# Optimization experiments

Hardware: AMD Instinct MI355X
Metric: run time of the kernel (lower is better)

## Reference

```python
import jax, jax.numpy as jnp
import numpy as np

B, S, D, H = 4, 2048, 1024, 16
HD = D // H
SCALE = D ** (-0.5)  # NOTE: original scales by embedding_dim**-0.5, not head_size**-0.5


def setup_inputs() -> dict:
    key = jax.random.key(0)
    k1, k2, k3, k4, k5 = jax.random.split(key, 5)
    return {
        "x": jax.random.normal(k1, (B, S, D), dtype=jnp.float32),
        "Wqkv": jax.random.normal(k2, (3 * D, D), dtype=jnp.float32) * (D ** -0.5),
        "bqkv": jax.random.normal(k3, (3 * D,), dtype=jnp.float32) * 0.02,
        "Wlift": jax.random.normal(k4, (D, D), dtype=jnp.float32) * (D ** -0.5),
        "blift": jax.random.normal(k5, (D,), dtype=jnp.float32) * 0.02,
    }


def reference(x, Wqkv, bqkv, Wlift, blift):
    b, s, d = x.shape
    # qkv projection -> (b, s, 3, H, HD) -> (3, b, H, s, HD)
    qkv = (x @ Wqkv.T + bqkv).reshape(b, s, 3, H, HD).transpose(2, 0, 3, 1, 4)
    q, k, v = qkv[0], qkv[1], qkv[2]  # each (b, H, s, HD)
    # full score matrix, softmax over keys
    scores = jnp.einsum("bhqd,bhkd->bhqk", q, k) * SCALE
    a = jax.nn.softmax(scores, axis=-1)
    # post-hoc causal mask + renormalize (as in the original)
    a = jnp.tril(a)
    a = a / jnp.sum(a, axis=-1, keepdims=True)
    attn = jnp.einsum("bhqk,bhkd->bhqd", a, v)  # (b, H, s, HD)
    attn = attn.swapaxes(1, 2).reshape(b, s, d)  # (b, s, d)
    # lifting linear; Dropout(0.2) is identity in eval mode
    return attn @ Wlift.T + blift
```

## Files before the change

kernel.cpp:

```cpp
#include <hip/hip_runtime.h>
#include <cstdint>
#include <cstddef>

typedef unsigned short u16;
typedef unsigned int u32;
typedef __bf16 bf16x8 __attribute__((ext_vector_type(8)));
typedef float f32x4 __attribute__((ext_vector_type(4)));
typedef float f32x16 __attribute__((ext_vector_type(16)));

__device__ __forceinline__ u16 f2bf(float f) {
  unsigned u = __builtin_bit_cast(unsigned, f);
  return (u16)((u + 0x7FFFu + ((u >> 16) & 1u)) >> 16);
}

__device__ __forceinline__ u32 pk2bf(float lo, float hi) {
  union { __bf16 h[2]; u32 u; } t;
  t.h[0] = (__bf16)lo; t.h[1] = (__bf16)hi;
  return t.u;
}

__device__ __forceinline__ void gl_lds16(const void* g, void* l) {
  __builtin_amdgcn_global_load_lds(
      (const __attribute__((address_space(1))) unsigned int*)g,
      (__attribute__((address_space(3))) unsigned int*)l,
      16, 0, 0);
}

__global__ void cast4_kernel(const float* __restrict__ in, u16* __restrict__ out, int n4) {
  int i = blockIdx.x * blockDim.x + threadIdx.x;
  if (i < n4) {
    float4 v = reinterpret_cast<const float4*>(in)[i];
    ushort4 o;
    o.x = f2bf(v.x); o.y = f2bf(v.y); o.z = f2bf(v.z); o.w = f2bf(v.w);
    reinterpret_cast<ushort4*>(out)[i] = o;
  }
}

template <int EPI>
__global__ __launch_bounds__(256)
void gemm_bt_kernel(const u16* __restrict__ A, const u16* __restrict__ Bw,
                    const float* __restrict__ bias,
                    u16* __restrict__ oq, u16* __restrict__ ok, u16* __restrict__ ovT,
                    float* __restrict__ ofp, int M, int N, int K) {
  __shared__ __align__(16) u16 Als[2][128 * 32];
  __shared__ __align__(16) u16 Bls[2][128 * 32];

  const int tid = threadIdx.x;
  const int lane = tid & 63;
  const int w = tid >> 6, wr = w >> 1, wc = w & 1;
  const int lr = lane & 15, lk = lane >> 4;
  const int brow = blockIdx.y * 128, bcol = blockIdx.x * 128;

  const int srow = tid >> 2;
  const int scol = (tid & 3) << 3;
  const u16* ga = A + (size_t)(brow + srow) * K + scol;
  const u16* gb = Bw + (size_t)(bcol + srow) * K + scol;

  f32x4 acc[4][4] = {};

  auto stage = [&](int buf, int kt) {
    const u16* a0 = ga + kt * 32;
    const u16* b0 = gb + kt * 32;
    gl_lds16(a0,             &Als[buf][tid * 8]);
    gl_lds16(a0 + 64 * K,    &Als[buf][2048 + tid * 8]);
    gl_lds16(b0,             &Bls[buf][tid * 8]);
    gl_lds16(b0 + 64 * K,    &Bls[buf][2048 + tid * 8]);
  };

  stage(0, 0);
  __syncthreads();

  const int nt = K >> 5;
  int cur = 0;
  for (int t = 0; t < nt; ++t) {
    if (t + 1 < nt) stage(cur ^ 1, t + 1);
    bf16x8 af[4], bfr[4];
#pragma unroll
    for (int m = 0; m < 4; ++m)
      af[m] = *reinterpret_cast<const bf16x8*>(&Als[cur][(wr * 64 + m * 16 + lr) * 32 + lk * 8]);
#pragma unroll
    for (int n = 0; n < 4; ++n)
      bfr[n] = *reinterpret_cast<const bf16x8*>(&Bls[cur][(wc * 64 + n * 16 + lr) * 32 + lk * 8]);
#pragma unroll
    for (int m = 0; m < 4; ++m)
#pragma unroll
      for (int n = 0; n < 4; ++n)
        acc[m][n] = __builtin_amdgcn_mfma_f32_16x16x32_bf16(af[m], bfr[n], acc[m][n], 0, 0, 0);
    __syncthreads();
    cur ^= 1;
  }

  if (EPI == 0) {
    const int three = bcol >> 10;
#pragma unroll
    for (int n = 0; n < 4; ++n) {
      const int c = bcol + wc * 64 + n * 16 + lr;
      const float bv = bias[c];
      const int cc = c & 1023, h = cc >> 6, hd = cc & 63;
#pragma unroll
      for (int m = 0; m < 4; ++m) {
        const int r0 = brow + wr * 64 + m * 16 + lk * 4;
        const int b = r0 >> 11;
        const int s0 = r0 & 2047;
        if (three == 2) {
          ushort4 pkv;
          pkv.x = f2bf(acc[m][n][0] + bv);
          pkv.y = f2bf(acc[m][n][1] + bv);
          pkv.z = f2bf(acc[m][n][2] + bv);
          pkv.w = f2bf(acc[m][n][3] + bv);
          *reinterpret_cast<ushort4*>(&ovT[((size_t)(b * 16 + h) * 64 + hd) * 2048 + s0]) = pkv;
        } else {
          u16* dst = (three == 0) ? oq : ok;
          const float sc = (three == 0) ? 0.03125f * 1.44269504089f : 1.0f;
#pragma unroll
          for (int j = 0; j < 4; ++j)
            dst[((size_t)(b * 16 + h) * 2048 + (s0 + j)) * 64 + hd] = f2bf((acc[m][n][j] + bv) * sc);
        }
      }
    }
  } else {
#pragma unroll
    for (int n = 0; n < 4; ++n) {
      const int c = bcol + wc * 64 + n * 16 + lr;
      const float bv = bias[c];
#pragma unroll
      for (int m = 0; m < 4; ++m) {
        const int r0 = brow + wr * 64 + m * 16 + lk * 4;
#pragma unroll
        for (int j = 0; j < 4; ++j)
          ofp[(size_t)(r0 + j) * N + c] = acc[m][n][j] + bv;
      }
    }
  }
}

__global__ __launch_bounds__(512, 4)
void attn_causal_kernel(const u16* __restrict__ qg, const u16* __restrict__ kg_,
                        const u16* __restrict__ vT, u16* __restrict__ ob) {
  __shared__ __align__(16) u16 Kls[2][64 * 64];
  __shared__ __align__(16) u16 Vls[2][64 * 64];

  const int tid = threadIdx.x, lane = tid & 63, w = tid >> 6;
  const int n = lane & 31, hi = lane >> 5;
  const int bid = blockIdx.x;
  const int bh = bid & 63;
  const int qb = (bid < 256) ? (7 - (bid >> 6)) : ((bid - 256) >> 6);
  const int q0w = qb * 256 + w * 32;
  const size_t base = (size_t)bh * 2048 * 64;
  const size_t vbase = (size_t)bh * 64 * 2048;

  bf16x8 qf[4];
#pragma unroll
  for (int dc = 0; dc < 4; ++dc)
    qf[dc] = *reinterpret_cast<const bf16x8*>(
        &qg[base + (size_t)(q0w + n) * 64 + dc * 16 + hi * 8]);

  f32x16 o0 = {}, o1 = {};
  float l = 0.f;

  const int ktiles = qb * 4 + 4;

  const int krow = tid >> 3, kch = tid & 7;
  const int szr = (krow ^ (krow >> 3)) & 7;
  const u16* kgp = kg_ + base + (size_t)krow * 64 + (kch ^ szr) * 8;
  const u16* vgp = vT + vbase + (size_t)krow * 2048 + (kch ^ szr) * 8;

  auto stage = [&](int buf, int t) {
    gl_lds16(kgp + (size_t)t * 4096, &Kls[buf][tid * 8]);
    gl_lds16(vgp + t * 64,           &Vls[buf][tid * 8]);
  };

  const int sw0 = ((n ^ (n >> 3)) & 7) << 4;
  const int sw1 = (((32 + n) ^ ((32 + n) >> 3)) & 7) << 4;

  stage(0, 0);
  __syncthreads();

  int cur = 0;
  for (int t = 0; t < ktiles; ++t) {
    const int k0 = t << 6;
    if (t + 1 < ktiles) stage(cur ^ 1, t + 1);
    if (k0 <= q0w) {
      const char* Kb = (const char*)&Kls[cur][0];
      const char* Vb = (const char*)&Vls[cur][0];
      const bool act1 = (k0 + 32) <= q0w;

      f32x16 st0 = {}, st1 = {};
      __builtin_amdgcn_s_setprio(1);
#pragma unroll
      for (int dc = 0; dc < 4; ++dc) {
        bf16x8 kf = *reinterpret_cast<const bf16x8*>(
            Kb + n * 128 + ((((dc << 1) | hi) << 4) ^ sw0));
        st0 = __builtin_amdgcn_mfma_f32_32x32x16_bf16(kf, qf[dc], st0, 0, 0, 0);
      }
      if (act1) {
#pragma unroll
        for (int dc = 0; dc < 4; ++dc) {
          bf16x8 kf = *reinterpret_cast<const bf16x8*>(
              Kb + (32 + n) * 128 + ((((dc << 1) | hi) << 4) ^ sw1));
          st1 = __builtin_amdgcn_mfma_f32_32x32x16_bf16(kf, qf[dc], st1, 0, 0, 0);
        }
      }
      __builtin_amdgcn_s_setprio(0);

      if (k0 == q0w) {
#pragma unroll
        for (int r = 0; r < 16; ++r) {
          const int koff = (r & 3) + 8 * (r >> 2) + 4 * hi;
          if (koff > n) st0[r] = -1e30f;
        }
      }
      if (act1 && (k0 + 32) == q0w) {
#pragma unroll
        for (int r = 0; r < 16; ++r) {
          const int koff = (r & 3) + 8 * (r >> 2) + 4 * hi;
          if (koff > n) st1[r] = -1e30f;
        }
      }

      float rs = 0.f;
#pragma unroll
      for (int r = 0; r < 16; ++r) { st0[r] = __builtin_amdgcn_exp2f(st0[r]); rs += st0[r]; }
      if (act1) {
#pragma unroll
        for (int r = 0; r < 16; ++r) { st1[r] = __builtin_amdgcn_exp2f(st1[r]); rs += st1[r]; }
      }
      l += rs;

      union { u32 u[4]; bf16x8 v; } pb[4];
#pragma unroll
      for (int s = 0; s < 2; ++s) {
        if (s == 1 && !act1) break;
        const f32x16& st = s ? st1 : st0;
#pragma unroll
        for (int kk = 0; kk < 2; ++kk) {
          const int gown = (kk * 2 + hi) * 4, gsnd = (kk * 2 + (hi ^ 1)) * 4;
          u32 pa0 = pk2bf(st[gown + 0], st[gown + 1]);
          u32 pa1 = pk2bf(st[gown + 2], st[gown + 3]);
          u32 ps0 = pk2bf(st[gsnd + 0], st[gsnd + 1]);
          u32 ps1 = pk2bf(st[gsnd + 2], st[gsnd + 3]);
          u32 rA = __shfl_xor(ps0, 32, 64);
          u32 rB = __shfl_xor(ps1, 32, 64);
          pb[s * 2 + kk].u[0] = hi ? rA : pa0;
          pb[s * 2 + kk].u[1] = hi ? rB : pa1;
          pb[s * 2 + kk].u[2] = hi ? pa0 : rA;
          pb[s * 2 + kk].u[3] = hi ? pa1 : rB;
        }
      }
      __builtin_amdgcn_s_setprio(1);
#pragma unroll
      for (int s = 0; s < 2; ++s) {
        if (s == 1 && !act1) break;
#pragma unroll
        for (int kk = 0; kk < 2; ++kk) {
          const int c = ((s * 4 + kk * 2 + hi) << 4);
          bf16x8 vf0 = *reinterpret_cast<const bf16x8*>(Vb + n * 128 + (c ^ sw0));
          o0 = __builtin_amdgcn_mfma_f32_32x32x16_bf16(vf0, pb[s * 2 + kk].v, o0, 0, 0, 0);
          bf16x8 vf1 = *reinterpret_cast<const bf16x8*>(Vb + (32 + n) * 128 + (c ^ sw1));
          o1 = __builtin_amdgcn_mfma_f32_32x32x16_bf16(vf1, pb[s * 2 + kk].v, o1, 0, 0, 0);
        }
      }
      __builtin_amdgcn_s_setprio(0);
    }
    __syncthreads();
    cur ^= 1;
  }

  const int b = bh >> 4, h = bh & 15;
  const float lt = l + __shfl_xor(l, 32, 64);
  const float inv = 1.f / lt;
  const size_t rbase = ((size_t)(b * 2048 + q0w + n)) * 1024 + h * 64;
#pragma unroll
  for (int g = 0; g < 4; ++g) {
    ushort4 w0, w1;
    w0.x = f2bf(o0[g * 4 + 0] * inv); w0.y = f2bf(o0[g * 4 + 1] * inv);
    w0.z = f2bf(o0[g * 4 + 2] * inv); w0.w = f2bf(o0[g * 4 + 3] * inv);
    w1.x = f2bf(o1[g * 4 + 0] * inv); w1.y = f2bf(o1[g * 4 + 1] * inv);
    w1.z = f2bf(o1[g * 4 + 2] * inv); w1.w = f2bf(o1[g * 4 + 3] * inv);
    *reinterpret_cast<ushort4*>(&ob[rbase + g * 8 + hi * 4]) = w0;
    *reinterpret_cast<ushort4*>(&ob[rbase + 32 + g * 8 + hi * 4]) = w1;
  }
}

extern "C" void kernel_launch(void* const* d_in, const int* in_sizes, int n_in,
                              void* d_out, int out_size, void* d_ws, size_t ws_size,
                              hipStream_t stream) {
  const float* x     = (const float*)d_in[0];
  const float* Wqkv  = (const float*)d_in[1];
  const float* bqkv  = (const float*)d_in[2];
  const float* Wlift = (const float*)d_in[3];
  const float* blift = (const float*)d_in[4];
  float* out = (float*)d_out;

  if (ws_size < 40ull * 1024 * 1024) return;

  char* ws = (char*)d_ws;
  u16* xb     = (u16*)(ws);
  u16* wqkvb  = (u16*)(ws + 16777216);
  u16* wliftb = (u16*)(ws + 23068672);
  u16* vT     = (u16*)(ws + 25165824);
  u16* attnb  = xb;
  u16* qb = (u16*)d_out;
  u16* kb = qb + 8388608;

  cast4_kernel<<<8192, 256, 0, stream>>>(x, xb, 2097152);
  cast4_kernel<<<3072, 256, 0, stream>>>(Wqkv, wqkvb, 786432);
  cast4_kernel<<<1024, 256, 0, stream>>>(Wlift, wliftb, 262144);

  gemm_bt_kernel<0><<<dim3(24, 64), 256, 0, stream>>>(
      xb, wqkvb, bqkv, qb, kb, vT, nullptr, 8192, 3072, 1024);

  attn_causal_kernel<<<512, 512, 0, stream>>>(qb, kb, vT, attnb);

  gemm_bt_kernel<1><<<dim3(8, 64), 256, 0, stream>>>(
      attnb, wliftb, blift, nullptr, nullptr, nullptr, out, 8192, 1024, 1024);
}
```

Baseline: 299.8 us.

## Stage K/V tiles through registers with two-ahead prefetch instead of direct-to-LDS loads

Replaces the direct global-to-LDS async copies of K and V tiles with ordinary global loads into registers, issued two tiles ahead. Each tile is written into the swizzled LDS slot after the current tile's compute finishes. The old __syncthreads becomes an explicit lgkmcnt wait, s_barrier and sched_barrier. The aim is to hide global-load latency behind more than one tile of MFMA work, at the cost of extra VGPRs for the staging buffers and explicit LDS stores on the critical path.

```diff
diff --git a/kernel.cpp b/kernel.cpp
--- a/kernel.cpp
+++ b/kernel.cpp
@@ -162,27 +162,35 @@
 
   const int krow = tid >> 3, kch = tid & 7;
   const int szr = (krow ^ (krow >> 3)) & 7;
-  const u16* kgp = kg_ + base + (size_t)krow * 64 + (kch ^ szr) * 8;
-  const u16* vgp = vT + vbase + (size_t)krow * 2048 + (kch ^ szr) * 8;
-
-  auto stage = [&](int buf, int t) {
-    gl_lds16(kgp + (size_t)t * 4096, &Kls[buf][tid * 8]);
-    gl_lds16(vgp + t * 64,           &Vls[buf][tid * 8]);
-  };
+  const u16* kgp = kg_ + base + (size_t)krow * 64 + kch * 8;
+  const u16* vgp = vT + vbase + (size_t)krow * 2048 + kch * 8;
+  u16* kwp = &Kls[0][krow * 64 + (kch ^ szr) * 8];
+  u16* vwp = &Vls[0][krow * 64 + (kch ^ szr) * 8];
+
+  int4 kst[2], vst[2];
+  kst[0] = *reinterpret_cast<const int4*>(kgp);
+  vst[0] = *reinterpret_cast<const int4*>(vgp);
+  kst[1] = *reinterpret_cast<const int4*>(kgp + 4096);
+  vst[1] = *reinterpret_cast<const int4*>(vgp + 64);
+  *reinterpret_cast<int4*>(kwp) = kst[0];
+  *reinterpret_cast<int4*>(vwp) = vst[0];
+  asm volatile("s_waitcnt lgkmcnt(0)" ::: "memory");
+  __builtin_amdgcn_s_barrier();
+  __builtin_amdgcn_sched_barrier(0);
 
   const int sw0 = ((n ^ (n >> 3)) & 7) << 4;
   const int sw1 = (((32 + n) ^ ((32 + n) >> 3)) & 7) << 4;
 
-  stage(0, 0);
-  __syncthreads();
-
-  int cur = 0;
   for (int t = 0; t < ktiles; ++t) {
     const int k0 = t << 6;
-    if (t + 1 < ktiles) stage(cur ^ 1, t + 1);
+    const int slot = t & 1;
+    if (t + 2 < ktiles) {
+      kst[slot] = *reinterpret_cast<const int4*>(kgp + (size_t)(t + 2) * 4096);
+      vst[slot] = *reinterpret_cast<const int4*>(vgp + (t + 2) * 64);
+    }
     if (k0 <= q0w) {
-      const char* Kb = (const char*)&Kls[cur][0];
-      const char* Vb = (const char*)&Vls[cur][0];
+      const char* Kb = (const char*)&Kls[slot][0];
+      const char* Vb = (const char*)&Vls[slot][0];
       const bool act1 = (k0 + 32) <= q0w;
 
       f32x16 st0 = {}, st1 = {};
@@ -262,8 +270,14 @@
       }
       __builtin_amdgcn_s_setprio(0);
     }
-    __syncthreads();
-    cur ^= 1;
+    if (t + 1 < ktiles) {
+      const int ws = (t + 1) & 1;
+      *reinterpret_cast<int4*>(kwp + ws * 4096) = kst[ws];
+      *reinterpret_cast<int4*>(vwp + ws * 4096) = vst[ws];
+    }
+    asm volatile("s_waitcnt lgkmcnt(0)" ::: "memory");
+    __builtin_amdgcn_s_barrier();
+    __builtin_amdgcn_sched_barrier(0);
   }
 
   const int b = bh >> 4, h = bh & 15;
```

Measured after the change: 324.5 us. 8.2% more time.

## Pair mirrored query strips per wave and stage K/V through registers

Applied to the files above, without the earlier changes.

Each wave now owns two 32-row query strips (j and 63-j), so every block does the same causal work. Each block streams all 32 K/V tiles once and shares them across both strips. The async global-to-LDS loads are replaced by register-staged loads with a two-deep prefetch and explicit barriers, and the block size drops from 512 to 256 threads. This targets load imbalance across blocks and K/V reload overhead, at the cost of more live registers (two Q fragment sets and accumulators) and lower per-block parallelism.

```diff
diff --git a/kernel.cpp b/kernel.cpp
--- a/kernel.cpp
+++ b/kernel.cpp
@@ -134,7 +134,7 @@
   }
 }
 
-__global__ __launch_bounds__(512, 4)
+__global__ __launch_bounds__(256, 2)
 void attn_causal_kernel(const u16* __restrict__ qg, const u16* __restrict__ kg_,
                         const u16* __restrict__ vT, u16* __restrict__ ob) {
   __shared__ __align__(16) u16 Kls[2][64 * 64];
@@ -144,142 +144,175 @@
   const int n = lane & 31, hi = lane >> 5;
   const int bid = blockIdx.x;
   const int bh = bid & 63;
-  const int qb = (bid < 256) ? (7 - (bid >> 6)) : ((bid - 256) >> 6);
-  const int q0w = qb * 256 + w * 32;
+  const int bq = bid >> 6;
+  const int jA = bq * 4 + w;
+  const int jB = 63 - jA;
+  const int q0A = jA * 32, q0B = jB * 32;
   const size_t base = (size_t)bh * 2048 * 64;
   const size_t vbase = (size_t)bh * 64 * 2048;
 
-  bf16x8 qf[4];
-#pragma unroll
-  for (int dc = 0; dc < 4; ++dc)
-    qf[dc] = *reinterpret_cast<const bf16x8*>(
-        &qg[base + (size_t)(q0w + n) * 64 + dc * 16 + hi * 8]);
-
-  f32x16 o0 = {}, o1 = {};
-  float l = 0.f;
-
-  const int ktiles = qb * 4 + 4;
-
-  const int krow = tid >> 3, kch = tid & 7;
-  const int szr = (krow ^ (krow >> 3)) & 7;
-  const u16* kgp = kg_ + base + (size_t)krow * 64 + (kch ^ szr) * 8;
-  const u16* vgp = vT + vbase + (size_t)krow * 2048 + (kch ^ szr) * 8;
-
-  auto stage = [&](int buf, int t) {
-    gl_lds16(kgp + (size_t)t * 4096, &Kls[buf][tid * 8]);
-    gl_lds16(vgp + t * 64,           &Vls[buf][tid * 8]);
-  };
+  bf16x8 qfA[4], qfB[4];
+#pragma unroll
+  for (int dc = 0; dc < 4; ++dc) {
+    qfA[dc] = *reinterpret_cast<const bf16x8*>(
+        &qg[base + (size_t)(q0A + n) * 64 + dc * 16 + hi * 8]);
+    qfB[dc] = *reinterpret_cast<const bf16x8*>(
+        &qg[base + (size_t)(q0B + n) * 64 + dc * 16 + hi * 8]);
+  }
+
+  f32x16 oA0 = {}, oA1 = {}, oB0 = {}, oB1 = {};
+  float lA = 0.f, lB = 0.f;
+
+  const int srow_ = tid >> 2;
+  const int sch = tid & 3;
+  const int ssz = (srow_ ^ (srow_ >> 3)) & 7;
+  const u16* kgp = kg_ + base + (size_t)srow_ * 64 + sch * 8;
+  const u16* vgp = vT + vbase + (size_t)srow_ * 2048 + sch * 8;
+  u16* kw0 = &Kls[0][srow_ * 64 + ((sch ^ ssz) * 8)];
+  u16* kw1 = &Kls[0][srow_ * 64 + (((sch + 4) ^ ssz) * 8)];
+  u16* vw0 = &Vls[0][srow_ * 64 + ((sch ^ ssz) * 8)];
+  u16* vw1 = &Vls[0][srow_ * 64 + (((sch + 4) ^ ssz) * 8)];
 
   const int sw0 = ((n ^ (n >> 3)) & 7) << 4;
   const int sw1 = (((32 + n) ^ ((32 + n) >> 3)) & 7) << 4;
 
-  stage(0, 0);
-  __syncthreads();
-
-  int cur = 0;
-  for (int t = 0; t < ktiles; ++t) {
-    const int k0 = t << 6;
-    if (t + 1 < ktiles) stage(cur ^ 1, t + 1);
-    if (k0 <= q0w) {
-      const char* Kb = (const char*)&Kls[cur][0];
-      const char* Vb = (const char*)&Vls[cur][0];
-      const bool act1 = (k0 + 32) <= q0w;
-
-      f32x16 st0 = {}, st1 = {};
+  struct Slot { int4 k0, k1, v0, v1; };
+  Slot sA, sB;
+
+  sA.k0 = *reinterpret_cast<const int4*>(kgp);
+  sA.k1 = *reinterpret_cast<const int4*>(kgp + 32);
+  sA.v0 = *reinterpret_cast<const int4*>(vgp);
+  sA.v1 = *reinterpret_cast<const int4*>(vgp + 32);
+  sB.k0 = *reinterpret_cast<const int4*>(kgp + 4096);
+  sB.k1 = *reinterpret_cast<const int4*>(kgp + 4096 + 32);
+  sB.v0 = *reinterpret_cast<const int4*>(vgp + 64);
+  sB.v1 = *reinterpret_cast<const int4*>(vgp + 64 + 32);
+  *reinterpret_cast<int4*>(kw0) = sA.k0;
+  *reinterpret_cast<int4*>(kw1) = sA.k1;
+  *reinterpret_cast<int4*>(vw0) = sA.v0;
+  *reinterpret_cast<int4*>(vw1) = sA.v1;
+  asm volatile("s_waitcnt lgkmcnt(0)" ::: "memory");
+  __builtin_amdgcn_s_barrier();
+  __builtin_amdgcn_sched_barrier(0);
+
+  auto slab_one = [&](const char* Kb, const char* Vb, int s, bool diag,
+                      const bf16x8 (&qf)[4], f32x16& o0, f32x16& o1, float& l) {
+    const int swK = s ? sw1 : sw0;
+    f32x16 st = {};
+    __builtin_amdgcn_s_setprio(1);
+#pragma unroll
+    for (int dc = 0; dc < 4; ++dc) {
+      bf16x8 kf = *reinterpret_cast<const bf16x8*>(
+          Kb + (s * 32 + n) * 128 + ((((dc << 1) | hi) << 4) ^ swK));
+      st = __builtin_amdgcn_mfma_f32_32x32x16_bf16(kf, qf[dc], st, 0, 0, 0);
+    }
+    __builtin_amdgcn_s_setprio(0);
+    if (diag) {
+#pragma unroll
+      for (int r = 0; r < 16; ++r) {
+        const int koff = (r & 3) + 8 * (r >> 2) + 4 * hi;
+        if (koff > n) st[r] = -1e30f;
+      }
+    }
+    float rs = 0.f;
+#pragma unroll
+    for (int r = 0; r < 16; ++r) { st[r] = __builtin_amdgcn_exp2f(st[r]); rs += st[r]; }
+    l += rs;
+#pragma unroll
+    for (int kk = 0; kk < 2; ++kk) {
+      const int gown = (kk * 2 + hi) * 4, gsnd = (kk * 2 + (hi ^ 1)) * 4;
+      u32 pa0 = pk2bf(st[gown + 0], st[gown + 1]);
+      u32 pa1 = pk2bf(st[gown + 2], st[gown + 3]);
+      u32 ps0 = pk2bf(st[gsnd + 0], st[gsnd + 1]);
+      u32 ps1 = pk2bf(st[gsnd + 2], st[gsnd + 3]);
+      u32 rA = __shfl_xor(ps0, 32, 64);
+      u32 rB = __shfl_xor(ps1, 32, 64);
+      union { u32 u[4]; bf16x8 v; } pb;
+      pb.u[0] = hi ? rA : pa0;
+      pb.u[1] = hi ? rB : pa1;
+      pb.u[2] = hi ? pa0 : rA;
+      pb.u[3] = hi ? pa1 : rB;
+      const int c = ((s * 4 + kk * 2 + hi) << 4);
       __builtin_amdgcn_s_setprio(1);
-#pragma unroll
-      for (int dc = 0; dc < 4; ++dc) {
-        bf16x8 kf = *reinterpret_cast<const bf16x8*>(
-            Kb + n * 128 + ((((dc << 1) | hi) << 4) ^ sw0));
-        st0 = __builtin_amdgcn_mfma_f32_32x32x16_bf16(kf, qf[dc], st0, 0, 0, 0);
-      }
-      if (act1) {
-#pragma unroll
-        for (int dc = 0; dc < 4; ++dc) {
-          bf16x8 kf = *reinterpret_cast<const bf16x8*>(
-              Kb + (32 + n) * 128 + ((((dc << 1) | hi) << 4) ^ sw1));
-          st1 = __builtin_amdgcn_mfma_f32_32x32x16_bf16(kf, qf[dc], st1, 0, 0, 0);
-        }
-      }
+      bf16x8 vf0 = *reinterpret_cast<const bf16x8*>(Vb + n * 128 + (c ^ sw0));
+      o0 = __builtin_amdgcn_mfma_f32_32x32x16_bf16(vf0, pb.v, o0, 0, 0, 0);
+      bf16x8 vf1 = *reinterpret_cast<const bf16x8*>(Vb + (32 + n) * 128 + (c ^ sw1));
+      o1 = __builtin_amdgcn_mfma_f32_32x32x16_bf16(vf1, pb.v, o1, 0, 0, 0);
       __builtin_amdgcn_s_setprio(0);
-
-      if (k0 == q0w) {
-#pragma unroll
-        for (int r = 0; r < 16; ++r) {
-          const int koff = (r & 3) + 8 * (r >> 2) + 4 * hi;
-          if (koff > n) st0[r] = -1e30f;
-        }
-      }
-      if (act1 && (k0 + 32) == q0w) {
-#pragma unroll
-        for (int r = 0; r < 16; ++r) {
-          const int koff = (r & 3) + 8 * (r >> 2) + 4 * hi;
-          if (koff > n) st1[r] = -1e30f;
-        }
-      }
-
-      float rs = 0.f;
-#pragma unroll
-      for (int r = 0; r < 16; ++r) { st0[r] = __builtin_amdgcn_exp2f(st0[r]); rs += st0[r]; }
-      if (act1) {
-#pragma unroll
-        for (int r = 0; r < 16; ++r) { st1[r] = __builtin_amdgcn_exp2f(st1[r]); rs += st1[r]; }
-      }
-      l += rs;
-
-      union { u32 u[4]; bf16x8 v; } pb[4];
-#pragma unroll
-      for (int s = 0; s < 2; ++s) {
-        if (s == 1 && !act1) break;
-        const f32x16& st = s ? st1 : st0;
-#pragma unroll
-        for (int kk = 0; kk < 2; ++kk) {
-          const int gown = (kk * 2 + hi) * 4, gsnd = (kk * 2 + (hi ^ 1)) * 4;
-          u32 pa0 = pk2bf(st[gown + 0], st[gown + 1]);
-          u32 pa1 = pk2bf(st[gown + 2], st[gown + 3]);
-          u32 ps0 = pk2bf(st[gsnd + 0], st[gsnd + 1]);
-          u32 ps1 = pk2bf(st[gsnd + 2], st[gsnd + 3]);
-          u32 rA = __shfl_xor(ps0, 32, 64);
-          u32 rB = __shfl_xor(ps1, 32, 64);
-          pb[s * 2 + kk].u[0] = hi ? rA : pa0;
-          pb[s * 2 + kk].u[1] = hi ? rB : pa1;
-          pb[s * 2 + kk].u[2] = hi ? pa0 : rA;
-          pb[s * 2 + kk].u[3] = hi ? pa1 : rB;
-        }
-      }
-      __builtin_amdgcn_s_setprio(1);
-#pragma unroll
-      for (int s = 0; s < 2; ++s) {
-        if (s == 1 && !act1) break;
-#pragma unroll
-        for (int kk = 0; kk < 2; ++kk) {
-          const int c = ((s * 4 + kk * 2 + hi) << 4);
-          bf16x8 vf0 = *reinterpret_cast<const bf16x8*>(Vb + n * 128 + (c ^ sw0));
-          o0 = __builtin_amdgcn_mfma_f32_32x32x16_bf16(vf0, pb[s * 2 + kk].v, o0, 0, 0, 0);
-          bf16x8 vf1 = *reinterpret_cast<const bf16x8*>(Vb + (32 + n) * 128 + (c ^ sw1));
-          o1 = __builtin_amdgcn_mfma_f32_32x32x16_bf16(vf1, pb[s * 2 + kk].v, o1, 0, 0, 0);
-        }
-      }
-      __builtin_amdgcn_s_setprio(0);
-    }
-    __syncthreads();
-    cur ^= 1;
+    }
+  };
+
+  auto tilecomp = [&](int t, const char* Kb, const char* Vb) {
+#pragma unroll
+    for (int s = 0; s < 2; ++s) {
+      const int e = 2 * t + s;
+      if (e <= jA) slab_one(Kb, Vb, s, e == jA, qfA, oA0, oA1, lA);
+      if (e <= jB) slab_one(Kb, Vb, s, e == jB, qfB, oB0, oB1, lB);
+    }
+  };
+
+  const char* K0 = (const char*)&Kls[0][0];
+  const char* V0 = (const char*)&Vls[0][0];
+  const char* K1 = (const char*)&Kls[1][0];
+  const char* V1 = (const char*)&Vls[1][0];
+
+  for (int tp = 0; tp < 16; ++tp) {
+    {
+      const int t = tp * 2;
+      if (t + 2 < 32) {
+        sA.k0 = *reinterpret_cast<const int4*>(kgp + (size_t)(t + 2) * 4096);
+        sA.k1 = *reinterpret_cast<const int4*>(kgp + (size_t)(t + 2) * 4096 + 32);
+        sA.v0 = *reinterpret_cast<const int4*>(vgp + (t + 2) * 64);
+        sA.v1 = *reinterpret_cast<const int4*>(vgp + (t + 2) * 64 + 32);
+      }
+      tilecomp(t, K0, V0);
+      *reinterpret_cast<int4*>(kw0 + 4096) = sB.k0;
+      *reinterpret_cast<int4*>(kw1 + 4096) = sB.k1;
+      *reinterpret_cast<int4*>(vw0 + 4096) = sB.v0;
+      *reinterpret_cast<int4*>(vw1 + 4096) = sB.v1;
+      asm volatile("s_waitcnt lgkmcnt(0)" ::: "memory");
+      __builtin_amdgcn_s_barrier();
+      __builtin_amdgcn_sched_barrier(0);
+    }
+    {
+      const int t = tp * 2 + 1;
+      if (t + 2 < 32) {
+        sB.k0 = *reinterpret_cast<const int4*>(kgp + (size_t)(t + 2) * 4096);
+        sB.k1 = *reinterpret_cast<const int4*>(kgp + (size_t)(t + 2) * 4096 + 32);
+        sB.v0 = *reinterpret_cast<const int4*>(vgp + (t + 2) * 64);
+        sB.v1 = *reinterpret_cast<const int4*>(vgp + (t + 2) * 64 + 32);
+      }
+      tilecomp(t, K1, V1);
+      if (t + 1 < 32) {
+        *reinterpret_cast<int4*>(kw0) = sA.k0;
+        *reinterpret_cast<int4*>(kw1) = sA.k1;
+        *reinterpret_cast<int4*>(vw0) = sA.v0;
+        *reinterpret_cast<int4*>(vw1) = sA.v1;
+      }
+      asm volatile("s_waitcnt lgkmcnt(0)" ::: "memory");
+      __builtin_amdgcn_s_barrier();
+      __builtin_amdgcn_sched_barrier(0);
+    }
   }
 
   const int b = bh >> 4, h = bh & 15;
-  const float lt = l + __shfl_xor(l, 32, 64);
-  const float inv = 1.f / lt;
-  const size_t rbase = ((size_t)(b * 2048 + q0w + n)) * 1024 + h * 64;
-#pragma unroll
-  for (int g = 0; g < 4; ++g) {
-    ushort4 w0, w1;
-    w0.x = f2bf(o0[g * 4 + 0] * inv); w0.y = f2bf(o0[g * 4 + 1] * inv);
-    w0.z = f2bf(o0[g * 4 + 2] * inv); w0.w = f2bf(o0[g * 4 + 3] * inv);
-    w1.x = f2bf(o1[g * 4 + 0] * inv); w1.y = f2bf(o1[g * 4 + 1] * inv);
-    w1.z = f2bf(o1[g * 4 + 2] * inv); w1.w = f2bf(o1[g * 4 + 3] * inv);
-    *reinterpret_cast<ushort4*>(&ob[rbase + g * 8 + hi * 4]) = w0;
-    *reinterpret_cast<ushort4*>(&ob[rbase + 32 + g * 8 + hi * 4]) = w1;
-  }
+  auto epi = [&](int q0, const f32x16& o0, const f32x16& o1, float l) {
+    const float lt = l + __shfl_xor(l, 32, 64);
+    const float inv = 1.f / lt;
+    const size_t rbase = ((size_t)(b * 2048 + q0 + n)) * 1024 + h * 64;
+#pragma unroll
+    for (int g = 0; g < 4; ++g) {
+      ushort4 w0, w1;
+      w0.x = f2bf(o0[g * 4 + 0] * inv); w0.y = f2bf(o0[g * 4 + 1] * inv);
+      w0.z = f2bf(o0[g * 4 + 2] * inv); w0.w = f2bf(o0[g * 4 + 3] * inv);
+      w1.x = f2bf(o1[g * 4 + 0] * inv); w1.y = f2bf(o1[g * 4 + 1] * inv);
+      w1.z = f2bf(o1[g * 4 + 2] * inv); w1.w = f2bf(o1[g * 4 + 3] * inv);
+      *reinterpret_cast<ushort4*>(&ob[rbase + g * 8 + hi * 4]) = w0;
+      *reinterpret_cast<ushort4*>(&ob[rbase + 32 + g * 8 + hi * 4]) = w1;
+    }
+  };
+  epi(q0A, oA0, oA1, lA);
+  epi(q0B, oB0, oB1, lB);
 }
 
 extern "C" void kernel_launch(void* const* d_in, const int* in_sizes, int n_in,
@@ -310,7 +343,7 @@
   gemm_bt_kernel<0><<<dim3(24, 64), 256, 0, stream>>>(
       xb, wqkvb, bqkv, qb, kb, vT, nullptr, 8192, 3072, 1024);
 
-  attn_causal_kernel<<<512, 512, 0, stream>>>(qb, kb, vT, attnb);
+  attn_causal_kernel<<<512, 256, 0, stream>>>(qb, kb, vT, attnb);
 
   gemm_bt_kernel<1><<<dim3(8, 64), 256, 0, stream>>>(
       attnb, wliftb, blift, nullptr, nullptr, nullptr, out, 8192, 1024, 1024);
```

Result: slower. 322.8 us (+7.7%).

## Pair complementary causal query tiles per wave for balanced attention work

Applied to the files above, without the earlier changes.

Each wave now owns two 32-row query tiles, jA and 63-jA, so every wave does the same amount of causal work. Blocks shrink to 256 threads, and each block now streams all 32 K/V tiles for its head. Loaded K fragments are reused across both query tiles' MFMAs. The cost is more registers for two sets of accumulators, and each block now reads the full K/V sequence.

```diff
diff --git a/kernel.cpp b/kernel.cpp
--- a/kernel.cpp
+++ b/kernel.cpp
@@ -134,7 +134,7 @@
   }
 }
 
-__global__ __launch_bounds__(512, 4)
+__global__ __launch_bounds__(256, 2)
 void attn_causal_kernel(const u16* __restrict__ qg, const u16* __restrict__ kg_,
                         const u16* __restrict__ vT, u16* __restrict__ ob) {
   __shared__ __align__(16) u16 Kls[2][64 * 64];
@@ -144,30 +144,38 @@
   const int n = lane & 31, hi = lane >> 5;
   const int bid = blockIdx.x;
   const int bh = bid & 63;
-  const int qb = (bid < 256) ? (7 - (bid >> 6)) : ((bid - 256) >> 6);
-  const int q0w = qb * 256 + w * 32;
+  const int bq = bid >> 6;
+  const int jA = bq * 4 + w;
+  const int jB = 63 - jA;
+  const int q0A = jA * 32, q0B = jB * 32;
   const size_t base = (size_t)bh * 2048 * 64;
   const size_t vbase = (size_t)bh * 64 * 2048;
 
-  bf16x8 qf[4];
-#pragma unroll
-  for (int dc = 0; dc < 4; ++dc)
-    qf[dc] = *reinterpret_cast<const bf16x8*>(
-        &qg[base + (size_t)(q0w + n) * 64 + dc * 16 + hi * 8]);
-
-  f32x16 o0 = {}, o1 = {};
-  float l = 0.f;
-
-  const int ktiles = qb * 4 + 4;
+  bf16x8 qfA[4], qfB[4];
+#pragma unroll
+  for (int dc = 0; dc < 4; ++dc) {
+    qfA[dc] = *reinterpret_cast<const bf16x8*>(
+        &qg[base + (size_t)(q0A + n) * 64 + dc * 16 + hi * 8]);
+    qfB[dc] = *reinterpret_cast<const bf16x8*>(
+        &qg[base + (size_t)(q0B + n) * 64 + dc * 16 + hi * 8]);
+  }
+
+  f32x16 oA0 = {}, oA1 = {}, oB0 = {}, oB1 = {};
+  float lA = 0.f, lB = 0.f;
 
   const int krow = tid >> 3, kch = tid & 7;
-  const int szr = (krow ^ (krow >> 3)) & 7;
-  const u16* kgp = kg_ + base + (size_t)krow * 64 + (kch ^ szr) * 8;
-  const u16* vgp = vT + vbase + (size_t)krow * 2048 + (kch ^ szr) * 8;
 
   auto stage = [&](int buf, int t) {
-    gl_lds16(kgp + (size_t)t * 4096, &Kls[buf][tid * 8]);
-    gl_lds16(vgp + t * 64,           &Vls[buf][tid * 8]);
+    const int k0 = t << 6;
+#pragma unroll
+    for (int p = 0; p < 2; ++p) {
+      const int r = p * 32 + krow;
+      const int sz = (r ^ (r >> 3)) & 7;
+      gl_lds16(kg_ + base + (size_t)(k0 + r) * 64 + (kch ^ sz) * 8,
+               &Kls[buf][p * 2048 + tid * 8]);
+      gl_lds16(vT + vbase + (size_t)r * 2048 + k0 + (kch ^ sz) * 8,
+               &Vls[buf][p * 2048 + tid * 8]);
+    }
   };
 
   const int sw0 = ((n ^ (n >> 3)) & 7) << 4;
@@ -176,110 +184,114 @@
   stage(0, 0);
   __syncthreads();
 
-  int cur = 0;
-  for (int t = 0; t < ktiles; ++t) {
-    const int k0 = t << 6;
-    if (t + 1 < ktiles) stage(cur ^ 1, t + 1);
-    if (k0 <= q0w) {
-      const char* Kb = (const char*)&Kls[cur][0];
-      const char* Vb = (const char*)&Vls[cur][0];
-      const bool act1 = (k0 + 32) <= q0w;
-
-      f32x16 st0 = {}, st1 = {};
+  union U { u32 u[4]; bf16x8 v; };
+
+  auto maskst = [&](f32x16& st) {
+#pragma unroll
+    for (int r = 0; r < 16; ++r) {
+      const int koff = (r & 3) + 8 * (r >> 2) + 4 * hi;
+      if (koff > n) st[r] = -1e30f;
+    }
+  };
+  auto packp = [&](const f32x16& st, int kk, U& pb) {
+    const int gown = (kk * 2 + hi) * 4, gsnd = (kk * 2 + (hi ^ 1)) * 4;
+    u32 pa0 = pk2bf(st[gown + 0], st[gown + 1]);
+    u32 pa1 = pk2bf(st[gown + 2], st[gown + 3]);
+    u32 ps0 = pk2bf(st[gsnd + 0], st[gsnd + 1]);
+    u32 ps1 = pk2bf(st[gsnd + 2], st[gsnd + 3]);
+    u32 rA = __shfl_xor(ps0, 32, 64);
+    u32 rB = __shfl_xor(ps1, 32, 64);
+    pb.u[0] = hi ? rA : pa0;
+    pb.u[1] = hi ? rB : pa1;
+    pb.u[2] = hi ? pa0 : rA;
+    pb.u[3] = hi ? pa1 : rB;
+  };
+
+  auto slab_pair = [&](const char* Kb, const char* Vb, int s,
+                       bool actA, bool actB, bool diagA, bool diagB) {
+    const int swK = s ? sw1 : sw0;
+    bf16x8 kf[4];
+#pragma unroll
+    for (int dc = 0; dc < 4; ++dc)
+      kf[dc] = *reinterpret_cast<const bf16x8*>(
+          Kb + (s * 32 + n) * 128 + ((((dc << 1) | hi) << 4) ^ swK));
+    f32x16 stA = {}, stB = {};
+    __builtin_amdgcn_s_setprio(1);
+#pragma unroll
+    for (int dc = 0; dc < 4; ++dc) {
+      if (actA) stA = __builtin_amdgcn_mfma_f32_32x32x16_bf16(kf[dc], qfA[dc], stA, 0, 0, 0);
+      if (actB) stB = __builtin_amdgcn_mfma_f32_32x32x16_bf16(kf[dc], qfB[dc], stB, 0, 0, 0);
+    }
+    __builtin_amdgcn_s_setprio(0);
+    if (diagA) maskst(stA);
+    if (diagB) maskst(stB);
+    if (actA) {
+      float rs = 0.f;
+#pragma unroll
+      for (int r = 0; r < 16; ++r) { stA[r] = __builtin_amdgcn_exp2f(stA[r]); rs += stA[r]; }
+      lA += rs;
+    }
+    if (actB) {
+      float rs = 0.f;
+#pragma unroll
+      for (int r = 0; r < 16; ++r) { stB[r] = __builtin_amdgcn_exp2f(stB[r]); rs += stB[r]; }
+      lB += rs;
+    }
+#pragma unroll
+    for (int kk = 0; kk < 2; ++kk) {
+      U pbA, pbB;
+      if (actA) packp(stA, kk, pbA);
+      if (actB) packp(stB, kk, pbB);
+      const int c = ((s * 4 + kk * 2 + hi) << 4);
+      bf16x8 vf0 = *reinterpret_cast<const bf16x8*>(Vb + n * 128 + (c ^ sw0));
+      bf16x8 vf1 = *reinterpret_cast<const bf16x8*>(Vb + (32 + n) * 128 + (c ^ sw1));
       __builtin_amdgcn_s_setprio(1);
-#pragma unroll
-      for (int dc = 0; dc < 4; ++dc) {
-        bf16x8 kf = *reinterpret_cast<const bf16x8*>(
-            Kb + n * 128 + ((((dc << 1) | hi) << 4) ^ sw0));
-        st0 = __builtin_amdgcn_mfma_f32_32x32x16_bf16(kf, qf[dc], st0, 0, 0, 0);
+      if (actA) {
+        oA0 = __builtin_amdgcn_mfma_f32_32x32x16_bf16(vf0, pbA.v, oA0, 0, 0, 0);
+        oA1 = __builtin_amdgcn_mfma_f32_32x32x16_bf16(vf1, pbA.v, oA1, 0, 0, 0);
       }
-      if (act1) {
-#pragma unroll
-        for (int dc = 0; dc < 4; ++dc) {
-          bf16x8 kf = *reinterpret_cast<const bf16x8*>(
-              Kb + (32 + n) * 128 + ((((dc << 1) | hi) << 4) ^ sw1));
-          st1 = __builtin_amdgcn_mfma_f32_32x32x16_bf16(kf, qf[dc], st1, 0, 0, 0);
-        }
+      if (actB) {
+        oB0 = __builtin_amdgcn_mfma_f32_32x32x16_bf16(vf0, pbB.v, oB0, 0, 0, 0);
+        oB1 = __builtin_amdgcn_mfma_f32_32x32x16_bf16(vf1, pbB.v, oB1, 0, 0, 0);
       }
       __builtin_amdgcn_s_setprio(0);
-
-      if (k0 == q0w) {
-#pragma unroll
-        for (int r = 0; r < 16; ++r) {
-          const int koff = (r & 3) + 8 * (r >> 2) + 4 * hi;
-          if (koff > n) st0[r] = -1e30f;
-        }
-      }
-      if (act1 && (k0 + 32) == q0w) {
-#pragma unroll
-        for (int r = 0; r < 16; ++r) {
-          const int koff = (r & 3) + 8 * (r >> 2) + 4 * hi;
-          if (koff > n) st1[r] = -1e30f;
-        }
-      }
-
-      float rs = 0.f;
-#pragma unroll
-      for (int r = 0; r < 16; ++r) { st0[r] = __builtin_amdgcn_exp2f(st0[r]); rs += st0[r]; }
-      if (act1) {
-#pragma unroll
-        for (int r = 0; r < 16; ++r) { st1[r] = __builtin_amdgcn_exp2f(st1[r]); rs += st1[r]; }
-      }
-      l += rs;
-
-      union { u32 u[4]; bf16x8 v; } pb[4];
-#pragma unroll
-      for (int s = 0; s < 2; ++s) {
-        if (s == 1 && !act1) break;
-        const f32x16& st = s ? st1 : st0;
-#pragma unroll
-        for (int kk = 0; kk < 2; ++kk) {
-          const int gown = (kk * 2 + hi) * 4, gsnd = (kk * 2 + (hi ^ 1)) * 4;
-          u32 pa0 = pk2bf(st[gown + 0], st[gown + 1]);
-          u32 pa1 = pk2bf(st[gown + 2], st[gown + 3]);
-          u32 ps0 = pk2bf(st[gsnd + 0], st[gsnd + 1]);
-          u32 ps1 = pk2bf(st[gsnd + 2], st[gsnd + 3]);
-          u32 rA = __shfl_xor(ps0, 32, 64);
-          u32 rB = __shfl_xor(ps1, 32, 64);
-          pb[s * 2 + kk].u[0] = hi ? rA : pa0;
-          pb[s * 2 + kk].u[1] = hi ? rB : pa1;
-          pb[s * 2 + kk].u[2] = hi ? pa0 : rA;
-          pb[s * 2 + kk].u[3] = hi ? pa1 : rB;
-        }
-      }
-      __builtin_amdgcn_s_setprio(1);
-#pragma unroll
-      for (int s = 0; s < 2; ++s) {
-        if (s == 1 && !act1) break;
-#pragma unroll
-        for (int kk = 0; kk < 2; ++kk) {
-          const int c = ((s * 4 + kk * 2 + hi) << 4);
-          bf16x8 vf0 = *reinterpret_cast<const bf16x8*>(Vb + n * 128 + (c ^ sw0));
-          o0 = __builtin_amdgcn_mfma_f32_32x32x16_bf16(vf0, pb[s * 2 + kk].v, o0, 0, 0, 0);
-          bf16x8 vf1 = *reinterpret_cast<const bf16x8*>(Vb + (32 + n) * 128 + (c ^ sw1));
-          o1 = __builtin_amdgcn_mfma_f32_32x32x16_bf16(vf1, pb[s * 2 + kk].v, o1, 0, 0, 0);
-        }
-      }
-      __builtin_amdgcn_s_setprio(0);
+    }
+  };
+
+  int cur = 0;
+  for (int t = 0; t < 32; ++t) {
+    if (t + 1 < 32) stage(cur ^ 1, t + 1);
+    const char* Kb = (const char*)&Kls[cur][0];
+    const char* Vb = (const char*)&Vls[cur][0];
+#pragma unroll
+    for (int s = 0; s < 2; ++s) {
+      const int e = 2 * t + s;
+      const bool aA = e <= jA, aB = e <= jB;
+      if (aA || aB)
+        slab_pair(Kb, Vb, s, aA, aB, e == jA, e == jB);
     }
     __syncthreads();
     cur ^= 1;
   }
 
   const int b = bh >> 4, h = bh & 15;
-  const float lt = l + __shfl_xor(l, 32, 64);
-  const float inv = 1.f / lt;
-  const size_t rbase = ((size_t)(b * 2048 + q0w + n)) * 1024 + h * 64;
-#pragma unroll
-  for (int g = 0; g < 4; ++g) {
-    ushort4 w0, w1;
-    w0.x = f2bf(o0[g * 4 + 0] * inv); w0.y = f2bf(o0[g * 4 + 1] * inv);
-    w0.z = f2bf(o0[g * 4 + 2] * inv); w0.w = f2bf(o0[g * 4 + 3] * inv);
-    w1.x = f2bf(o1[g * 4 + 0] * inv); w1.y = f2bf(o1[g * 4 + 1] * inv);
-    w1.z = f2bf(o1[g * 4 + 2] * inv); w1.w = f2bf(o1[g * 4 + 3] * inv);
-    *reinterpret_cast<ushort4*>(&ob[rbase + g * 8 + hi * 4]) = w0;
-    *reinterpret_cast<ushort4*>(&ob[rbase + 32 + g * 8 + hi * 4]) = w1;
-  }
+  auto epi = [&](int q0, const f32x16& o0, const f32x16& o1, float l) {
+    const float lt = l + __shfl_xor(l, 32, 64);
+    const float inv = 1.f / lt;
+    const size_t rbase = ((size_t)(b * 2048 + q0 + n)) * 1024 + h * 64;
+#pragma unroll
+    for (int g = 0; g < 4; ++g) {
+      ushort4 w0, w1;
+      w0.x = f2bf(o0[g * 4 + 0] * inv); w0.y = f2bf(o0[g * 4 + 1] * inv);
+      w0.z = f2bf(o0[g * 4 + 2] * inv); w0.w = f2bf(o0[g * 4 + 3] * inv);
+      w1.x = f2bf(o1[g * 4 + 0] * inv); w1.y = f2bf(o1[g * 4 + 1] * inv);
+      w1.z = f2bf(o1[g * 4 + 2] * inv); w1.w = f2bf(o1[g * 4 + 3] * inv);
+      *reinterpret_cast<ushort4*>(&ob[rbase + g * 8 + hi * 4]) = w0;
+      *reinterpret_cast<ushort4*>(&ob[rbase + 32 + g * 8 + hi * 4]) = w1;
+    }
+  };
+  epi(q0A, oA0, oA1, lA);
+  epi(q0B, oB0, oB1, lB);
 }
 
 extern "C" void kernel_launch(void* const* d_in, const int* in_sizes, int n_in,
@@ -310,7 +322,7 @@
   gemm_bt_kernel<0><<<dim3(24, 64), 256, 0, stream>>>(
       xb, wqkvb, bqkv, qb, kb, vT, nullptr, 8192, 3072, 1024);
 
-  attn_causal_kernel<<<512, 512, 0, stream>>>(qb, kb, vT, attnb);
+  attn_causal_kernel<<<512, 256, 0, stream>>>(qb, kb, vT, attnb);
 
   gemm_bt_kernel<1><<<dim3(8, 64), 256, 0, stream>>>(
       attnb, wliftb, blift, nullptr, nullptr, nullptr, out, 8192, 1024, 1024);
```

Measured after the change: 295.6 us. About the same (-1.4%).
